# Optimization experiments

Hardware: AMD Instinct MI355X
Metric: run time of the kernel (lower is better)

The kernel has to match this reference:

```python
import jax, jax.numpy as jnp
import numpy as np

N_EMBD = 1024
N_HEADS = 16
HEAD_DIM = N_EMBD // N_HEADS


def setup_inputs() -> dict:
    key = jax.random.key(0)
    ks = jax.random.split(key, 12)
    B, T, S, C = 2, 2048, 2048, N_EMBD
    std = 1.0 / np.sqrt(C)
    inp = {
        "x": jax.random.normal(ks[0], (B, T, C), dtype=jnp.float32),
        "context": jax.random.normal(ks[1], (B, S, C), dtype=jnp.float32),
        "q_w": jax.random.uniform(ks[2], (C, C), minval=-std, maxval=std, dtype=jnp.float32),
        "q_b": jax.random.uniform(ks[3], (C,), minval=-std, maxval=std, dtype=jnp.float32),
        "k_w": jax.random.uniform(ks[4], (C, C), minval=-std, maxval=std, dtype=jnp.float32),
        "k_b": jax.random.uniform(ks[5], (C,), minval=-std, maxval=std, dtype=jnp.float32),
        "v_w": jax.random.uniform(ks[6], (C, C), minval=-std, maxval=std, dtype=jnp.float32),
        "v_b": jax.random.uniform(ks[7], (C,), minval=-std, maxval=std, dtype=jnp.float32),
        "o_w": jax.random.uniform(ks[8], (C, C), minval=-std, maxval=std, dtype=jnp.float32),
        "o_b": jax.random.uniform(ks[9], (C,), minval=-std, maxval=std, dtype=jnp.float32),
    }
    return inp


def reference(x, context, q_w, q_b, k_w, k_b, v_w, v_b, o_w, o_b):
    B, T, C = x.shape
    S = context.shape[1]
    H, D = N_HEADS, HEAD_DIM
    # projections (torch Linear: y = x @ W^T + b; here weights stored as [in, out])
    q = (x @ q_w + q_b).reshape(B, T, H, D).transpose(0, 2, 1, 3)        # [B,H,T,D]
    k = (context @ k_w + k_b).reshape(B, S, H, D).transpose(0, 2, 1, 3)  # [B,H,S,D]
    v = (context @ v_w + v_b).reshape(B, S, H, D).transpose(0, 2, 1, 3)  # [B,H,S,D]
    att = jnp.einsum("bhtd,bhsd->bhts", q, k) / jnp.sqrt(jnp.float32(D))  # [B,H,T,S]
    causal = jnp.tril(jnp.ones((T, S), dtype=bool))                       # mask from tril buffer
    att = jnp.where(causal[None, None, :, :], att, -jnp.inf)
    att = jax.nn.softmax(att, axis=-1)
    y = jnp.einsum("bhts,bhsd->bhtd", att, v)                             # [B,H,T,D]
    y = y.transpose(0, 2, 1, 3).reshape(B, T, C)
    return y @ o_w + o_b
```

## Files before the change

### kernel.cpp

```cpp
#include <hip/hip_runtime.h>
#include <hip/hip_bf16.h>

using bf16 = __bf16;
using bf16x4 = __attribute__((ext_vector_type(4))) __bf16;
using bf16x8 = __attribute__((ext_vector_type(8))) __bf16;
using f32x4 = __attribute__((ext_vector_type(4))) float;

#define EXP2F(x) __builtin_amdgcn_exp2f(x)

__global__ __launch_bounds__(256) void transpose_kernel(const float* __restrict__ w0,
                                                        const float* __restrict__ w1,
                                                        const float* __restrict__ w2,
                                                        const float* __restrict__ w3,
                                                        bf16* __restrict__ wtbase) {
  __shared__ float tile[32][33];
  const int z = blockIdx.z;
  const float* w = (z == 0) ? w0 : (z == 1) ? w1 : (z == 2) ? w2 : w3;
  bf16* wt = wtbase + (size_t)z * 1048576;
  int k0 = blockIdx.y * 32, n0 = blockIdx.x * 32;
  int tx = threadIdx.x, ty = threadIdx.y;
#pragma unroll
  for (int i = 0; i < 4; i++)
    tile[ty + i * 8][tx] = w[(size_t)(k0 + ty + i * 8) * 1024 + n0 + tx];
  __syncthreads();
#pragma unroll
  for (int i = 0; i < 4; i++)
    wt[(size_t)(n0 + ty + i * 8) * 1024 + k0 + tx] = (bf16)tile[tx][ty + i * 8];
}

template <int MODE, bool AF32>
__device__ __forceinline__ void gemm_body(char* __restrict__ smem,
                                          const void* __restrict__ Ap,
                                          const bf16* __restrict__ Bt,
                                          const float* __restrict__ bias,
                                          void* __restrict__ outp, int bx, int by,
                                          float oscale) {
  constexpr int K = 1024;
  bf16(*As)[40] = (bf16(*)[40])smem;
  bf16(*Bs)[40] = (bf16(*)[40])(smem + 10240);
  bf16(*Cs)[136] = (bf16(*)[136])smem;

  const int tid = threadIdx.x;
  const int lane = tid & 63;
  const int w = tid >> 6;
  const int wr = w >> 1, wc = w & 1;
  const int m0 = by * 128, n0 = bx * 128;
  const int fr = lane & 15, fg = (lane >> 4) * 8;

  f32x4 acc[4][4] = {};

  const int srow = tid >> 2;
  const int kc = (tid & 3) * 8;
  const int arow = m0 + srow, brow = n0 + srow;

  auto loadA = [&](int row, int kcol) -> bf16x8 {
    if constexpr (AF32) {
      const float* Af = (const float*)Ap;
      float4 u = *(const float4*)&Af[(size_t)row * K + kcol];
      float4 v = *(const float4*)&Af[(size_t)row * K + kcol + 4];
      bf16x8 r = {(bf16)u.x, (bf16)u.y, (bf16)u.z, (bf16)u.w,
                  (bf16)v.x, (bf16)v.y, (bf16)v.z, (bf16)v.w};
      return r;
    } else {
      const bf16* Ab = (const bf16*)Ap;
      return *(const bf16x8*)&Ab[(size_t)row * K + kcol];
    }
  };

  bf16x8 ra0, ra1, rb0, rb1;
  ra0 = loadA(arow, kc);
  ra1 = loadA(arow + 64, kc);
  rb0 = *(const bf16x8*)&Bt[(size_t)brow * K + kc];
  rb1 = *(const bf16x8*)&Bt[(size_t)(brow + 64) * K + kc];

  for (int k0 = 0; k0 < K; k0 += 32) {
    __syncthreads();
    *(bf16x8*)&As[srow][kc] = ra0;
    *(bf16x8*)&As[srow + 64][kc] = ra1;
    *(bf16x8*)&Bs[srow][kc] = rb0;
    *(bf16x8*)&Bs[srow + 64][kc] = rb1;
    if (k0 + 32 < K) {
      int kn = k0 + 32 + kc;
      ra0 = loadA(arow, kn);
      ra1 = loadA(arow + 64, kn);
      rb0 = *(const bf16x8*)&Bt[(size_t)brow * K + kn];
      rb1 = *(const bf16x8*)&Bt[(size_t)(brow + 64) * K + kn];
    }
    __syncthreads();
    bf16x8 af[4], bfr[4];
#pragma unroll
    for (int mi = 0; mi < 4; mi++)
      af[mi] = *(const bf16x8*)&As[wr * 64 + mi * 16 + fr][fg];
#pragma unroll
    for (int ni = 0; ni < 4; ni++)
      bfr[ni] = *(const bf16x8*)&Bs[wc * 64 + ni * 16 + fr][fg];
#pragma unroll
    for (int mi = 0; mi < 4; mi++)
#pragma unroll
      for (int ni = 0; ni < 4; ni++)
        acc[mi][ni] =
            __builtin_amdgcn_mfma_f32_16x16x32_bf16(af[mi], bfr[ni], acc[mi][ni], 0, 0, 0);
  }

  float bv[4];
#pragma unroll
  for (int ni = 0; ni < 4; ni++) bv[ni] = bias[n0 + wc * 64 + ni * 16 + fr];
#pragma unroll
  for (int mi = 0; mi < 4; mi++)
#pragma unroll
    for (int ni = 0; ni < 4; ni++)
#pragma unroll
      for (int j = 0; j < 4; j++) acc[mi][ni][j] = (acc[mi][ni][j] + bv[ni]) * oscale;

  if (MODE == 2) {
    float* O = (float*)outp;
#pragma unroll
    for (int mi = 0; mi < 4; mi++)
#pragma unroll
      for (int ni = 0; ni < 4; ni++)
#pragma unroll
        for (int j = 0; j < 4; j++) {
          int row = m0 + wr * 64 + mi * 16 + (lane >> 4) * 4 + j;
          int col = n0 + wc * 64 + ni * 16 + fr;
          O[(size_t)row * 1024 + col] = acc[mi][ni][j];
        }
    return;
  }

  __syncthreads();
#pragma unroll
  for (int mi = 0; mi < 4; mi++) {
    int r = wr * 64 + mi * 16 + (lane >> 4) * 4;
#pragma unroll
    for (int ni = 0; ni < 4; ni++) {
      int c = wc * 64 + ni * 16 + fr;
#pragma unroll
      for (int j = 0; j < 4; j++) Cs[r + j][c] = (bf16)acc[mi][ni][j];
    }
  }
  __syncthreads();

  bf16* O = (bf16*)outp;
  if (MODE == 0) {
    int row = tid >> 1, ch = (tid & 1) * 64;
    int rg = m0 + row;
    int b = rg >> 11, t_ = rg & 2047;
    int c0 = n0 + ch;
    int h = c0 >> 6;
    bf16* dst = O + ((size_t)(b * 16 + h) * 2048 + t_) * 64;
#pragma unroll
    for (int i = 0; i < 8; i++) *(bf16x8*)&dst[i * 8] = *(const bf16x8*)&Cs[row][ch + i * 8];
  } else {
    int colL = tid >> 1, sh = (tid & 1) * 64;
    int cg = n0 + colL;
    int h = cg >> 6, d = cg & 63;
    int rg = m0 + sh;
    int b = rg >> 11, s_ = rg & 2047;
    bf16* dst = O + ((size_t)((b * 16 + h) * 64 + d)) * 2048 + s_;
#pragma unroll
    for (int i = 0; i < 8; i++) {
      bf16x8 v;
#pragma unroll
      for (int jj = 0; jj < 8; jj++) v[jj] = Cs[sh + i * 8 + jj][colL];
      *(bf16x8*)&dst[i * 8] = v;
    }
  }
}

__global__ __launch_bounds__(256) void gemm_qkv_kernel(const float* __restrict__ x,
                                                       const float* __restrict__ ctx,
                                                       const bf16* __restrict__ wtbase,
                                                       const float* __restrict__ bq,
                                                       const float* __restrict__ bk,
                                                       const float* __restrict__ bv,
                                                       bf16* __restrict__ outbase) {
  __shared__ __align__(16) char smem[34816];
  const int lin = blockIdx.x;
  const int xcd = lin & 7, idx = lin >> 3;
  const int seq = xcd * 96 + idx;
  const int z = seq >> 8;
  const int rem = seq & 255;
  const int by = rem >> 3, bx = rem & 7;
  const float* A = (z == 0) ? x : ctx;
  const bf16* Wt = wtbase + (size_t)z * 1048576;
  const float* bias = (z == 0) ? bq : (z == 1) ? bk : bv;
  bf16* out = outbase + (size_t)z * 4194304;
  const float oscale = (z == 0) ? 0.125f * 1.4426950408889634f : 1.0f;
  if (z == 2)
    gemm_body<1, true>(smem, A, Wt, bias, (void*)out, bx, by, oscale);
  else
    gemm_body<0, true>(smem, A, Wt, bias, (void*)out, bx, by, oscale);
}

__global__ __launch_bounds__(256) void gemm_o_kernel(const bf16* __restrict__ A,
                                                     const bf16* __restrict__ Wt,
                                                     const float* __restrict__ bias,
                                                     float* __restrict__ out) {
  __shared__ __align__(16) char smem[34816];
  const int lin = blockIdx.x;
  const int xcd = lin & 7, idx = lin >> 3;
  const int seq = xcd * 32 + idx;
  const int by = seq >> 3, bx = seq & 7;
  gemm_body<2, false>(smem, A, Wt, bias, (void*)out, bx, by, 1.0f);
}

__global__ __launch_bounds__(256) void attn_kernel(const bf16* __restrict__ Q,
                                                   const bf16* __restrict__ Kc,
                                                   const bf16* __restrict__ Vt,
                                                   bf16* __restrict__ Y) {
  const int bh = blockIdx.x;
  const int qt = 31 - blockIdx.y;
  const int tid = threadIdx.x, lane = tid & 63, w = tid >> 6;
  const int lr = lane & 15, lg = lane >> 4;
  const int q0 = qt * 64 + w * 16;

  __shared__ __align__(16) bf16 Ks[64 * 64];
  __shared__ __align__(16) bf16 Vs[64 * 64];
  __shared__ __align__(16) bf16 Plds[4][16][72];

  const bf16* qb = Q + ((size_t)bh * 2048 + q0 + lr) * 64 + lg * 8;
  const bf16x8 qfB0 = *(const bf16x8*)qb;
  const bf16x8 qfB1 = *(const bf16x8*)(qb + 32);

  const bf16* Kbase = Kc + (size_t)bh * 2048 * 64;
  const bf16* Vbase = Vt + (size_t)bh * 64 * 2048;

  const int srow = tid >> 2;
  const int scol = (tid & 3) * 16;
  const int r7x = (srow & 7) * 8;
  const int d0 = srow * 64 + (scol ^ r7x);
  const int d1 = srow * 64 + ((scol + 8) ^ r7x);

  bf16x8 kr0, kr1, vr0, vr1;
  {
    const bf16* kp = Kbase + (size_t)srow * 64 + scol;
    kr0 = *(const bf16x8*)kp;
    kr1 = *(const bf16x8*)(kp + 8);
    const bf16* vp = Vbase + (size_t)srow * 2048 + scol;
    vr0 = *(const bf16x8*)vp;
    vr1 = *(const bf16x8*)(vp + 8);
  }

  f32x4 yacc[4] = {};
  float mrow = -__builtin_inff(), lrow = 0.0f;
  const int kxor = (lr & 7) * 8;

  for (int c = 0; c <= qt; ++c) {
    const int sbase = c * 64;
    __syncthreads();
    *(bf16x8*)&Ks[d0] = kr0;
    *(bf16x8*)&Ks[d1] = kr1;
    *(bf16x8*)&Vs[d0] = vr0;
    *(bf16x8*)&Vs[d1] = vr1;
    __syncthreads();

    {
      const int cn = (c < qt) ? c + 1 : c;
      const int sb = cn * 64;
      const bf16* kp = Kbase + (size_t)(sb + srow) * 64 + scol;
      kr0 = *(const bf16x8*)kp;
      kr1 = *(const bf16x8*)(kp + 8);
      const bf16* vp = Vbase + (size_t)srow * 2048 + sb + scol;
      vr0 = *(const bf16x8*)vp;
      vr1 = *(const bf16x8*)(vp + 8);
    }

    f32x4 st[4];
#pragma unroll
    for (int h = 0; h < 4; ++h) {
      const int rb = (16 * h + lr) * 64;
      const bf16x8 kf0 = *(const bf16x8*)&Ks[rb + ((lg * 8) ^ kxor)];
      const bf16x8 kf1 = *(const bf16x8*)&Ks[rb + ((32 + lg * 8) ^ kxor)];
      f32x4 z = {};
      z = __builtin_amdgcn_mfma_f32_16x16x32_bf16(kf0, qfB0, z, 0, 0, 0);
      z = __builtin_amdgcn_mfma_f32_16x16x32_bf16(kf1, qfB1, z, 0, 0, 0);
      st[h] = z;
    }
    if (c == qt) {
      const int qg = q0 + lr;
#pragma unroll
      for (int h = 0; h < 4; ++h)
#pragma unroll
        for (int j = 0; j < 4; ++j) {
          int sg = sbase + 16 * h + lg * 4 + j;
          if (sg > qg) st[h][j] = -__builtin_inff();
        }
    }
    float vmax = fmaxf(fmaxf(st[0][0], st[0][1]), fmaxf(st[0][2], st[0][3]));
#pragma unroll
    for (int h = 1; h < 4; ++h)
      vmax = fmaxf(vmax, fmaxf(fmaxf(st[h][0], st[h][1]), fmaxf(st[h][2], st[h][3])));
    vmax = fmaxf(vmax, __shfl_xor(vmax, 16));
    vmax = fmaxf(vmax, __shfl_xor(vmax, 32));

    if (!__all(vmax <= mrow)) {
      const float mnew = fmaxf(mrow, vmax);
      const float cf = EXP2F(mrow - mnew);
      mrow = mnew;
      lrow *= cf;
      float cfj[4];
#pragma unroll
      for (int j = 0; j < 4; ++j) cfj[j] = __shfl(cf, lg * 4 + j);
#pragma unroll
      for (int nf = 0; nf < 4; ++nf)
#pragma unroll
        for (int j = 0; j < 4; ++j) yacc[nf][j] *= cfj[j];
    }

    float rs = 0.0f;
#pragma unroll
    for (int h = 0; h < 4; ++h) {
      float p0 = EXP2F(st[h][0] - mrow);
      float p1 = EXP2F(st[h][1] - mrow);
      float p2 = EXP2F(st[h][2] - mrow);
      float p3 = EXP2F(st[h][3] - mrow);
      rs += (p0 + p1) + (p2 + p3);
      bf16x4 pk = {(bf16)p0, (bf16)p1, (bf16)p2, (bf16)p3};
      *(bf16x4*)&Plds[w][lr][16 * h + lg * 4] = pk;
    }
    rs += __shfl_xor(rs, 16);
    rs += __shfl_xor(rs, 32);
    lrow += rs;

    const bf16x8 pa0 = *(const bf16x8*)&Plds[w][lr][lg * 8];
    const bf16x8 pa1 = *(const bf16x8*)&Plds[w][lr][32 + lg * 8];
#pragma unroll
    for (int nf = 0; nf < 4; ++nf) {
      const int rb = (nf * 16 + lr) * 64;
      const bf16x8 vf0 = *(const bf16x8*)&Vs[rb + ((lg * 8) ^ kxor)];
      const bf16x8 vf1 = *(const bf16x8*)&Vs[rb + ((32 + lg * 8) ^ kxor)];
      yacc[nf] = __builtin_amdgcn_mfma_f32_16x16x32_bf16(pa0, vf0, yacc[nf], 0, 0, 0);
      yacc[nf] = __builtin_amdgcn_mfma_f32_16x16x32_bf16(pa1, vf1, yacc[nf], 0, 0, 0);
    }
  }

  const float rinv = 1.0f / lrow;
  float linv[4];
#pragma unroll
  for (int j = 0; j < 4; ++j) linv[j] = __shfl(rinv, lg * 4 + j);
  const int b = bh >> 4, h = bh & 15;
#pragma unroll
  for (int nf = 0; nf < 4; ++nf)
#pragma unroll
    for (int j = 0; j < 4; ++j) {
      int qg = q0 + lg * 4 + j;
      Y[((size_t)b * 2048 + qg) * 1024 + h * 64 + nf * 16 + lr] = (bf16)(yacc[nf][j] * linv[j]);
    }
}

extern "C" void kernel_launch(void* const* d_in, const int* in_sizes, int n_in,
                              void* d_out, int out_size, void* d_ws, size_t ws_size,
                              hipStream_t stream) {
  const float* x = (const float*)d_in[0];
  const float* ctx = (const float*)d_in[1];
  const float* q_w = (const float*)d_in[2];
  const float* q_b = (const float*)d_in[3];
  const float* k_w = (const float*)d_in[4];
  const float* k_b = (const float*)d_in[5];
  const float* v_w = (const float*)d_in[6];
  const float* v_b = (const float*)d_in[7];
  const float* o_w = (const float*)d_in[8];
  const float* o_b = (const float*)d_in[9];

  char* ws = (char*)d_ws;
  const size_t MB = 1024 * 1024;
  bf16* qwt = (bf16*)(ws + 0);
  bf16* Qws = (bf16*)(ws + 8 * MB);
  bf16* Kws = (bf16*)(ws + 16 * MB);
  bf16* Vt = (bf16*)(ws + 24 * MB);
  bf16* Yws = (bf16*)(ws + 32 * MB);
  bf16* owt = qwt + 3 * 1048576;

  dim3 tb(32, 8), tg(32, 32, 4);
  transpose_kernel<<<tg, tb, 0, stream>>>(q_w, k_w, v_w, o_w, qwt);

  gemm_qkv_kernel<<<768, 256, 0, stream>>>(x, ctx, qwt, q_b, k_b, v_b, Qws);

  attn_kernel<<<dim3(32, 32), 256, 0, stream>>>(Qws, Kws, Vt, Yws);

  gemm_o_kernel<<<256, 256, 0, stream>>>(Yws, owt, o_b, (float*)d_out);
}
```

Measured before the change: 115.1 us.

## Deepen GEMM register prefetch to two stages and raise wave priority around MFMAs

The GEMM main loop now keeps two sets of prefetch registers, so global loads for the k-tile two steps ahead are in flight while the current tile is computed. The goal is to hide more global-memory latency. In the attention kernel, s_setprio brackets the QK and PV MFMA blocks so waves issuing matrix ops are scheduled ahead of others. This costs extra VGPRs, which may reduce occupancy, and the priority hints may have little effect.

```diff
diff --git a/kernel.cpp b/kernel.cpp
--- a/kernel.cpp
+++ b/kernel.cpp
@@ -66,40 +66,56 @@
       return *(const bf16x8*)&Ab[(size_t)row * K + kcol];
     }
   };
-
-  bf16x8 ra0, ra1, rb0, rb1;
-  ra0 = loadA(arow, kc);
-  ra1 = loadA(arow + 64, kc);
-  rb0 = *(const bf16x8*)&Bt[(size_t)brow * K + kc];
-  rb1 = *(const bf16x8*)&Bt[(size_t)(brow + 64) * K + kc];
-
-  for (int k0 = 0; k0 < K; k0 += 32) {
-    __syncthreads();
-    *(bf16x8*)&As[srow][kc] = ra0;
-    *(bf16x8*)&As[srow + 64][kc] = ra1;
-    *(bf16x8*)&Bs[srow][kc] = rb0;
-    *(bf16x8*)&Bs[srow + 64][kc] = rb1;
-    if (k0 + 32 < K) {
-      int kn = k0 + 32 + kc;
-      ra0 = loadA(arow, kn);
-      ra1 = loadA(arow + 64, kn);
-      rb0 = *(const bf16x8*)&Bt[(size_t)brow * K + kn];
-      rb1 = *(const bf16x8*)&Bt[(size_t)(brow + 64) * K + kn];
-    }
-    __syncthreads();
-    bf16x8 af[4], bfr[4];
-#pragma unroll
-    for (int mi = 0; mi < 4; mi++)
-      af[mi] = *(const bf16x8*)&As[wr * 64 + mi * 16 + fr][fg];
-#pragma unroll
-    for (int ni = 0; ni < 4; ni++)
-      bfr[ni] = *(const bf16x8*)&Bs[wc * 64 + ni * 16 + fr][fg];
-#pragma unroll
-    for (int mi = 0; mi < 4; mi++)
+  auto loadT = [&](int kcol, bf16x8& ra0, bf16x8& ra1, bf16x8& rb0, bf16x8& rb1) {
+    ra0 = loadA(arow, kcol);
+    ra1 = loadA(arow + 64, kcol);
+    rb0 = *(const bf16x8*)&Bt[(size_t)brow * K + kcol];
+    rb1 = *(const bf16x8*)&Bt[(size_t)(brow + 64) * K + kcol];
+  };
+
+  bf16x8 ra0A, ra1A, rb0A, rb1A, ra0B, ra1B, rb0B, rb1B;
+  loadT(kc, ra0A, ra1A, rb0A, rb1A);
+  loadT(kc + 32, ra0B, ra1B, rb0B, rb1B);
+
+  for (int k0 = 0; k0 < K; k0 += 64) {
+#pragma unroll
+    for (int half = 0; half < 2; ++half) {
+      __syncthreads();
+      if (half == 0) {
+        *(bf16x8*)&As[srow][kc] = ra0A;
+        *(bf16x8*)&As[srow + 64][kc] = ra1A;
+        *(bf16x8*)&Bs[srow][kc] = rb0A;
+        *(bf16x8*)&Bs[srow + 64][kc] = rb1A;
+      } else {
+        *(bf16x8*)&As[srow][kc] = ra0B;
+        *(bf16x8*)&As[srow + 64][kc] = ra1B;
+        *(bf16x8*)&Bs[srow][kc] = rb0B;
+        *(bf16x8*)&Bs[srow + 64][kc] = rb1B;
+      }
+      __syncthreads();
+      {
+        const int kn = k0 + half * 32 + 64;
+        if (kn < K) {
+          if (half == 0)
+            loadT(kn + kc, ra0A, ra1A, rb0A, rb1A);
+          else
+            loadT(kn + kc, ra0B, ra1B, rb0B, rb1B);
+        }
+      }
+      bf16x8 af[4], bfr[4];
+#pragma unroll
+      for (int mi = 0; mi < 4; mi++)
+        af[mi] = *(const bf16x8*)&As[wr * 64 + mi * 16 + fr][fg];
 #pragma unroll
       for (int ni = 0; ni < 4; ni++)
-        acc[mi][ni] =
-            __builtin_amdgcn_mfma_f32_16x16x32_bf16(af[mi], bfr[ni], acc[mi][ni], 0, 0, 0);
+        bfr[ni] = *(const bf16x8*)&Bs[wc * 64 + ni * 16 + fr][fg];
+#pragma unroll
+      for (int mi = 0; mi < 4; mi++)
+#pragma unroll
+        for (int ni = 0; ni < 4; ni++)
+          acc[mi][ni] =
+              __builtin_amdgcn_mfma_f32_16x16x32_bf16(af[mi], bfr[ni], acc[mi][ni], 0, 0, 0);
+    }
   }
 
   float bv[4];
@@ -266,6 +282,7 @@
     }
 
     f32x4 st[4];
+    __builtin_amdgcn_s_setprio(1);
 #pragma unroll
     for (int h = 0; h < 4; ++h) {
       const int rb = (16 * h + lr) * 64;
@@ -276,6 +293,7 @@
       z = __builtin_amdgcn_mfma_f32_16x16x32_bf16(kf1, qfB1, z, 0, 0, 0);
       st[h] = z;
     }
+    __builtin_amdgcn_s_setprio(0);
     if (c == qt) {
       const int qg = q0 + lr;
 #pragma unroll
@@ -324,6 +342,7 @@
 
     const bf16x8 pa0 = *(const bf16x8*)&Plds[w][lr][lg * 8];
     const bf16x8 pa1 = *(const bf16x8*)&Plds[w][lr][32 + lg * 8];
+    __builtin_amdgcn_s_setprio(1);
 #pragma unroll
     for (int nf = 0; nf < 4; ++nf) {
       const int rb = (nf * 16 + lr) * 64;
@@ -332,6 +351,7 @@
       yacc[nf] = __builtin_amdgcn_mfma_f32_16x16x32_bf16(pa0, vf0, yacc[nf], 0, 0, 0);
       yacc[nf] = __builtin_amdgcn_mfma_f32_16x16x32_bf16(pa1, vf1, yacc[nf], 0, 0, 0);
     }
+    __builtin_amdgcn_s_setprio(0);
   }
 
   const float rinv = 1.0f / lrow;
```

Result: slower. 133.8 us (+16.2%).
